# Kernel tuning notes

Measured on AMD Instinct MI355X. Metric: run time of the kernel, lower is better.

The kernel has to match this reference:

```python
import jax, jax.numpy as jnp
import numpy as np

WS = 7       # window_size
SS = 3       # shift_size
HEADS = 6
HD = 32      # head_dim
DIM = 192    # embedding_dim
MLP_RATIO = 4
SCALE = HD ** -0.5
MM = WS * WS
NEG = -1e9


def _rel_index():
    # Swin relative-position index, shape [MM, MM], values in [0, (2*WS-1)^2)
    coords = np.stack(np.meshgrid(np.arange(WS), np.arange(WS), indexing='ij')).reshape(2, -1)
    rel = coords[:, :, None] - coords[:, None, :]          # [2, MM, MM]
    rel = rel.transpose(1, 2, 0).astype(np.int64)          # [MM, MM, 2]
    rel[:, :, 0] += WS - 1
    rel[:, :, 1] += WS - 1
    rel[:, :, 0] *= 2 * WS - 1
    return rel.sum(-1)                                     # [MM, MM]


def _shift_mask(h, w):
    # attention mask for shifted windows, shape [nh*nw, MM, MM]
    img = np.zeros((h, w), dtype=np.float32)
    cnt = 0
    for hs in (slice(0, -WS), slice(-WS, -SS), slice(-SS, None)):
        for ws_ in (slice(0, -WS), slice(-WS, -SS), slice(-SS, None)):
            img[hs, ws_] = cnt
            cnt += 1
    mw = img.reshape(h // WS, WS, w // WS, WS).transpose(0, 2, 1, 3).reshape(-1, MM)
    diff = mw[:, None, :] - mw[:, :, None]
    return np.where(diff != 0, NEG, 0.0).astype(np.float32)


def _ln(x, g, b):
    m = x.mean(-1, keepdims=True)
    v = ((x - m) ** 2).mean(-1, keepdims=True)
    return (x - m) / jnp.sqrt(v + 1e-5) * g + b


def setup_inputs() -> dict:
    key = jax.random.key(0)
    ks = jax.random.split(key, 8)
    inner = HEADS * HD

    def n(k, shape, s=0.02):
        return jax.random.normal(k, shape, jnp.float32) * s

    return {
        'x': jax.random.normal(ks[0], (64, DIM, 56, 56), jnp.float32),
        'ln1_g': jnp.ones((DIM,), jnp.float32),
        'ln1_b': jnp.zeros((DIM,), jnp.float32),
        'qkv_w': n(ks[1], (3 * inner, DIM)),
        'out_w': n(ks[2], (DIM, inner)),
        'out_b': jnp.zeros((DIM,), jnp.float32),
        'ln2_g': jnp.ones((DIM,), jnp.float32),
        'ln2_b': jnp.zeros((DIM,), jnp.float32),
        'mlp_w1': n(ks[3], (MLP_RATIO * DIM, DIM)),
        'mlp_b1': jnp.zeros((MLP_RATIO * DIM,), jnp.float32),
        'mlp_w2': n(ks[4], (DIM, MLP_RATIO * DIM)),
        'mlp_b2': jnp.zeros((DIM,), jnp.float32),
        'rel_table': n(ks[5], ((2 * WS - 1) ** 2, HEADS)),
    }


def reference(x, ln1_g, ln1_b, qkv_w, out_w, out_b, ln2_g, ln2_b,
              mlp_w1, mlp_b1, mlp_w2, mlp_b2, rel_table):
    b, c, h, w = x.shape
    nh, nw = h // WS, w // WS

    # cyclic shift
    xs = jnp.roll(x, (-SS, -SS), axis=(2, 3))
    # window partition: [b,c,h,w] -> [b*nh*nw, MM, c]
    xw = (xs.reshape(b, c, nh, WS, nw, WS)
            .transpose(0, 2, 4, 3, 5, 1)
            .reshape(b * nh * nw, MM, c))

    # --- attention (PreNorm) ---
    y = _ln(xw, ln1_g, ln1_b)
    qkv = y @ qkv_w.T                                 # [Bw, MM, 3*inner]
    q, k, v = jnp.split(qkv, 3, axis=-1)

    def to_heads(t):
        return t.reshape(-1, MM, HEADS, HD).transpose(0, 2, 1, 3)  # [Bw,H,MM,HD]

    q, k, v = to_heads(q), to_heads(k), to_heads(v)
    logits = jnp.einsum('bhid,bhjd->bhij', q, k) * SCALE           # [Bw,H,MM,MM]

    idx = jnp.asarray(_rel_index())
    bias = rel_table[idx.reshape(-1)].reshape(MM, MM, HEADS).transpose(2, 0, 1)  # [H,MM,MM]
    smask = jnp.asarray(_shift_mask(h, w))                         # [nh*nw,MM,MM]

    logits = (logits.reshape(b, nh * nw, HEADS, MM, MM)
              + bias[None, None] + smask[None, :, None])
    attn = jax.nn.softmax(logits, axis=-1).reshape(b * nh * nw, HEADS, MM, MM)
    o = jnp.einsum('bhij,bhjd->bhid', attn, v)                     # [Bw,H,MM,HD]
    o = o.transpose(0, 2, 1, 3).reshape(-1, MM, HEADS * HD)
    xw = xw + o @ out_w.T + out_b

    # --- MLP (PreNorm) ---
    y = _ln(xw, ln2_g, ln2_b)
    xw = xw + jax.nn.gelu(y @ mlp_w1.T + mlp_b1, approximate=False) @ mlp_w2.T + mlp_b2

    # window reverse + reverse shift
    xr = (xw.reshape(b, nh, nw, WS, WS, c)
            .transpose(0, 5, 1, 3, 2, 4)
            .reshape(b, c, h, w))
    return jnp.roll(xr, (SS, SS), axis=(2, 3))
```

## Files before the change

### kernel.cpp

```cpp
#include <hip/hip_runtime.h>
#include <hip/hip_bf16.h>
#include <hip/hip_fp8.h>

typedef unsigned short u16;
typedef unsigned int u32;
typedef unsigned char u8;
typedef __attribute__((ext_vector_type(4))) float fx4;
typedef __attribute__((ext_vector_type(8))) __bf16 bf8;

#define NEGV -1e9f
#define LOG2E 1.4426950408889634f
#define SCALE2 (0.17677669529663687f*1.4426950408889634f)

static __device__ __forceinline__ u16 f2bu(float f){
    __hip_bfloat16 h = __float2bfloat16(f);
    return *reinterpret_cast<u16*>(&h);
}
static __device__ __forceinline__ float b2f(u16 u){
    __hip_bfloat16 h;
    *reinterpret_cast<u16*>(&h) = u;
    return __bfloat162float(h);
}
static __device__ __forceinline__ u8 f2f8(float v){
    __hip_fp8_e4m3 t(v);
    return *reinterpret_cast<u8*>(&t);
}
static __device__ __forceinline__ float frcp(float x){
#if __has_builtin(__builtin_amdgcn_rcpf)
    return __builtin_amdgcn_rcpf(x);
#else
    return 1.f/x;
#endif
}
static __device__ __forceinline__ float frsq(float x){
#if __has_builtin(__builtin_amdgcn_rsqf)
    return __builtin_amdgcn_rsqf(x);
#else
    return rsqrtf(x);
#endif
}
static __device__ __forceinline__ float gelu_f(float v){
    return v * frcp(1.f + __builtin_amdgcn_exp2f(-2.4554418f*v));
}

__global__ __launch_bounds__(256) void f2b2_kernel(
        const float* __restrict__ s1, const float* __restrict__ s3,
        u16* __restrict__ d1, u8* __restrict__ d3){
    int i = blockIdx.x*256 + threadIdx.x;
    if (i < 36864)  d1[i] = f2bu(s1[i]);
    if (i < 147456) d3[i] = f2f8(s3[i]*16.f);
}

__global__ __launch_bounds__(256) void wprep_kernel(
        const float* __restrict__ qkv_w, const float* __restrict__ g1, const float* __restrict__ b1,
        const float* __restrict__ w1,    const float* __restrict__ g2, const float* __restrict__ b2,
        const float* __restrict__ mb1,
        u16* __restrict__ WqP, float* __restrict__ wsq, float* __restrict__ ccq,
        u16* __restrict__ W1P, float* __restrict__ ws1, float* __restrict__ cc1){
    const int row = blockIdx.x*4 + (threadIdx.x>>6);
    const int l = threadIdx.x & 63;
    const int isq = row < 576;
    const int n = isq ? row : row - 576;
    if (row >= 1344) return;
    const float* src = (isq ? qkv_w : w1) + (size_t)n*192;
    const float* g = isq ? g1 : g2;
    const float* b = isq ? b1 : b2;
    u16* dst = (isq ? WqP : W1P) + (size_t)n*192;
    float sw = 0.f, sc = 0.f;
    #pragma unroll
    for (int t=0;t<3;t++){
        const int k = l + t*64;
        const float wv = src[k];
        const float wp = wv*g[k];
        dst[k] = f2bu(wp);
        sw += wp; sc += b[k]*wv;
    }
    #pragma unroll
    for (int o=32;o;o>>=1){ sw += __shfl_xor(sw,o,64); sc += __shfl_xor(sc,o,64); }
    if (!l){
        if (isq){ wsq[n]=sw; ccq[n]=sc; }
        else    { ws1[n]=sw; cc1[n]=sc + mb1[n]; }
    }
}

__global__ __launch_bounds__(256) void ltab_kernel(const float* __restrict__ rel_table,
                                                   float* __restrict__ LT){
    const int blk = blockIdx.x;
    const int cls = blk/6, h = blk - cls*6;
    float* T = LT + blk*4096;
    for (int e = threadIdx.x; e < 4096; e += 256){
        const int i = e>>6, j = e&63;
        float v = NEGV;
        if (i < 49 && j < 49){
            const int id = i/7, im = i-id*7, jd = j/7, jm = j-jd*7;
            const int ridx = (id-jd+6)*13 + (im-jm+6);
            const float bias = rel_table[ridx*6 + h];
            const int ri = (cls&2) ? (id<4?1:2) : 0;
            const int rj = (cls&2) ? (jd<4?1:2) : 0;
            const int ci = (cls&1) ? (im<4?1:2) : 0;
            const int cj = (cls&1) ? (jm<4?1:2) : 0;
            v = bias + ((ri==rj && ci==cj) ? 0.f : NEGV);
        }
        T[e] = v * LOG2E;
    }
}

__global__ __launch_bounds__(256) void partition_ln_kernel(
        const float* __restrict__ x, u16* __restrict__ xw, float2* __restrict__ RS1){
    __shared__ float lds[192*57];
    const int bi = blockIdx.x;
    const int b = bi/56, i = bi%56;
    const int si = (i+3)%56;
    const float* src = x + (size_t)b*602112 + (size_t)si*56;
    for (int e = threadIdx.x; e < 10752; e += 256){
        int c = e/56, j = e%56;
        lds[c*57 + j] = src[(size_t)c*3136 + j];
    }
    __syncthreads();
    const int wrow_base = (b*8 + i/7)*8;
    const int prow = (i%7)*7;
    for (int e = threadIdx.x; e < 10752; e += 256){
        int j = e/192, c = e%192;
        int t = (wrow_base + j/7)*49 + prow + (j%7);
        xw[(size_t)t*192 + c] = f2bu(lds[c*57 + (j+3)%56]);
    }
    const int wv = threadIdx.x>>6, l = threadIdx.x&63;
    for (int j = wv; j < 56; j += 4){
        const int jj = (j+3)%56;
        float v0 = lds[l*57 + jj], v1 = lds[(l+64)*57 + jj], v2 = lds[(l+128)*57 + jj];
        float s = v0+v1+v2;
        #pragma unroll
        for (int o=32;o;o>>=1) s += __shfl_xor(s, o, 64);
        const float mean = s*(1.f/192.f);
        float d0 = v0-mean, d1 = v1-mean, d2 = v2-mean;
        float qv = d0*d0 + d1*d1 + d2*d2;
        #pragma unroll
        for (int o=32;o;o>>=1) qv += __shfl_xor(qv, o, 64);
        const float rstd = frsq(qv*(1.f/192.f) + 1e-5f);
        if (l == 0){
            const int t = (wrow_base + j/7)*49 + prow + (j%7);
            RS1[t] = make_float2(mean, rstd);
        }
    }
}

__global__ __launch_bounds__(256) void reverse_kernel(const u16* __restrict__ xw, float* __restrict__ out){
    __shared__ float lds[192*57];
    const int bi = blockIdx.x;
    const int b = bi/56, h = bi%56;
    const int i = (h+53)%56;
    const int wrow_base = (b*8 + i/7)*8;
    const int prow = (i%7)*7;
    for (int e = threadIdx.x; e < 10752; e += 256){
        int j = e/192, c = e%192;
        int t = (wrow_base + j/7)*49 + prow + (j%7);
        lds[c*57 + j] = b2f(xw[(size_t)t*192 + c]);
    }
    __syncthreads();
    float* dst = out + (size_t)b*602112 + (size_t)h*56;
    for (int e = threadIdx.x; e < 10752; e += 256){
        int c = e/56, w = e%56;
        dst[(size_t)c*3136 + w] = lds[c*57 + (w+53)%56];
    }
}

template<int ROWS>
static __device__ __forceinline__ void stage_tile(const char* __restrict__ g, size_t row0,
                                                  int kc, int pitch, u16* ldsbase, int tid){
    const int w = tid>>6, lane = tid&63;
    const int sub = lane>>3;
    const int b16 = (lane&7) ^ sub;
    #pragma unroll
    for (int i=0; i<ROWS/32; ++i){
        const int row = i*32 + w*8 + sub;
        const char* src = g + (row0+row)*(size_t)pitch + (size_t)kc*128 + b16*16;
        u16* dst = ldsbase + i*2048 + w*512;
#if __has_builtin(__builtin_amdgcn_global_load_lds)
        __builtin_amdgcn_global_load_lds(
            (const __attribute__((address_space(1))) u32*)src,
            (__attribute__((address_space(3))) u32*)dst, 16, 0, 0);
#else
        *(uint4*)(dst + lane*8) = *(const uint4*)src;
#endif
    }
}

static __device__ __forceinline__ bf8 rd_frag16(const u16* lds, int row, int boff){
    const char* p = (const char*)lds + row*128 + (boff ^ ((row&7)<<4));
    return *(const bf8*)p;
}
static __device__ __forceinline__ long rd_frag8(const u16* lds, int row, int boff){
    const char* p = (const char*)lds + row*128 + (boff ^ ((row&7)<<4));
    return *(const long*)p;
}

template<int KEL,int ESZ,int NY,int NTOT,int ACT,int RES,int LNF,int STATS,int OUT,int HASB>
__global__ __launch_bounds__(256,2) void gemm_kernel(
    const void* __restrict__ Av, const void* __restrict__ Bv,
    const float* __restrict__ bias, const u16* __restrict__ res,
    void* __restrict__ out,
    const float2* __restrict__ RSin, const float* __restrict__ wsum,
    const float* __restrict__ cc, float2* __restrict__ RSout,
    float ascale)
{
    constexpr int NKT = (KEL*ESZ)/128;
    constexpr int KKS = (ESZ==1)?4:2;
    constexpr int PITCH = KEL*ESZ;
    __shared__ __align__(16) u16 lds[40960];
    const int tid = threadIdx.x;
    const int wv = tid>>6, l = tid&63, lr = l&15, lg = l>>4;
    const int wm = wv&1, wn = wv>>1;
    const int chunk = gridDim.x >> 3;
    const int orig = (blockIdx.x & 7)*chunk + (blockIdx.x >> 3);
    const int mt = orig / NY;
    const int nc = orig - mt*NY;
    const size_t row0 = (size_t)mt*128;
    const int n0 = nc*192;
    const char* A = (const char*)Av;
    const char* Bblk = (const char*)Bv + (size_t)n0*PITCH;

    stage_tile<128>(A, row0, 0, PITCH, lds, tid);
    stage_tile<192>(Bblk, 0, 0, PITCH, lds+16384, tid);
    __syncthreads();

    fx4 acc[4][6] = {};
    for (int kc=0; kc<NKT; ++kc){
        const int cur = kc & 1;
        u16* Ac = cur ? (u16*)lds+8192  : (u16*)lds;
        u16* Bc = cur ? (u16*)lds+28672 : (u16*)lds+16384;
        if (kc+1 < NKT){
            u16* An = cur ? (u16*)lds       : (u16*)lds+8192;
            u16* Bn = cur ? (u16*)lds+16384 : (u16*)lds+28672;
            stage_tile<128>(A, row0, kc+1, PITCH, An, tid);
            stage_tile<192>(Bblk, 0, kc+1, PITCH, Bn, tid);
        }
        #pragma unroll
        for (int kk=0; kk<KKS; ++kk){
            if constexpr (ESZ==2){
                bf8 af[4], bfr[6];
                #pragma unroll
                for (int r=0;r<4;r++) af[r]  = rd_frag16(Ac, wm*64 + r*16 + lr, kk*64 + lg*16);
                #pragma unroll
                for (int c=0;c<6;c++) bfr[c] = rd_frag16(Bc, wn*96 + c*16 + lr, kk*64 + lg*16);
                #pragma unroll
                for (int r=0;r<4;r++)
                    #pragma unroll
                    for (int c=0;c<6;c++)
                        acc[r][c] = __builtin_amdgcn_mfma_f32_16x16x32_bf16(af[r], bfr[c], acc[r][c], 0,0,0);
            } else {
                long af[4], bfr[6];
                #pragma unroll
                for (int r=0;r<4;r++) af[r]  = rd_frag8(Ac, wm*64 + r*16 + lr, kk*32 + lg*8);
                #pragma unroll
                for (int c=0;c<6;c++) bfr[c] = rd_frag8(Bc, wn*96 + c*16 + lr, kk*32 + lg*8);
                #pragma unroll
                for (int r=0;r<4;r++)
                    #pragma unroll
                    for (int c=0;c<6;c++)
                        acc[r][c] = __builtin_amdgcn_mfma_f32_16x16x32_fp8_fp8(af[r], bfr[c], acc[r][c], 0,0,0);
            }
        }
        __syncthreads();
    }

    float sA[4][4], sB[4][4];
    if constexpr (LNF){
        #pragma unroll
        for (int r=0;r<4;r++)
            #pragma unroll
            for (int q=0;q<4;q++){
                const float2 st = RSin[row0 + wm*64 + r*16 + lg*4 + q];
                sA[r][q] = st.y;
                sB[r][q] = -st.x*st.y;
            }
    }
    float ss[4][4], ss2[4][4];
    if constexpr (STATS){
        #pragma unroll
        for (int r=0;r<4;r++)
            #pragma unroll
            for (int q=0;q<4;q++){ ss[r][q]=0.f; ss2[r][q]=0.f; }
    }
    #pragma unroll
    for (int c=0;c<6;c++){
        const int col = n0 + wn*96 + c*16 + lr;
        float bv = 0.f, wsc = 0.f, ccc = 0.f;
        if constexpr (HASB) bv = bias[col];
        if constexpr (LNF){ wsc = wsum[col]; ccc = cc[col]; }
        #pragma unroll
        for (int r=0;r<4;r++){
            const size_t grow0 = row0 + wm*64 + r*16 + lg*4;
            float vq[4];
            #pragma unroll
            for (int q=0;q<4;q++){
                float v = acc[r][c][q];
                if constexpr (ESZ==1) v *= ascale;
                if constexpr (LNF) v = fmaf(v, sA[r][q], fmaf(sB[r][q], wsc, ccc));
                else v += bv;
                if constexpr (ACT) v = gelu_f(v);
                if constexpr (RES) v += b2f(res[(grow0+q)*NTOT + col]);
                if constexpr (STATS){ ss[r][q] += v; ss2[r][q] += v*v; }
                vq[q] = v;
            }
            if constexpr (OUT==1){
                u16* ob = (u16*)out + grow0*NTOT + col;
                ob[0] = f2bu(vq[0]);
                ob[NTOT] = f2bu(vq[1]);
                ob[2*NTOT] = f2bu(vq[2]);
                ob[3*NTOT] = f2bu(vq[3]);
            } else {
                u8* ob = (u8*)out + grow0*(size_t)NTOT + col;
#if __has_builtin(__builtin_amdgcn_cvt_pk_fp8_f32)
                const u32 p01 = (u32)__builtin_amdgcn_cvt_pk_fp8_f32(vq[0], vq[1], 0, false);
                const u32 p23 = (u32)__builtin_amdgcn_cvt_pk_fp8_f32(vq[2], vq[3], 0, false);
                ob[0] = (u8)p01;
                ob[NTOT] = (u8)(p01>>8);
                ob[2*NTOT] = (u8)p23;
                ob[3*NTOT] = (u8)(p23>>8);
#else
                ob[0] = f2f8(vq[0]);
                ob[NTOT] = f2f8(vq[1]);
                ob[2*NTOT] = f2f8(vq[2]);
                ob[3*NTOT] = f2f8(vq[3]);
#endif
            }
        }
    }
    if constexpr (STATS){
        float* redS = (float*)lds;
        #pragma unroll
        for (int r=0;r<4;r++)
            #pragma unroll
            for (int q=0;q<4;q++){
                float s = ss[r][q], s2 = ss2[r][q];
                #pragma unroll
                for (int o=8;o;o>>=1){ s += __shfl_xor(s, o, 64); s2 += __shfl_xor(s2, o, 64); }
                if (lr == 0){
                    const int rowl = wm*64 + r*16 + lg*4 + q;
                    redS[(wn*128 + rowl)*2 + 0] = s;
                    redS[(wn*128 + rowl)*2 + 1] = s2;
                }
            }
        __syncthreads();
        for (int row = tid; row < 128; row += 256){
            const float S  = redS[row*2+0] + redS[(128+row)*2+0];
            const float S2 = redS[row*2+1] + redS[(128+row)*2+1];
            const float mean = S*(1.f/192.f);
            const float rstd = frsq(S2*(1.f/192.f) - mean*mean + 1e-5f);
            RSout[row0 + row] = make_float2(mean, rstd);
        }
    }
}

__global__ __launch_bounds__(64) void attn_kernel(const u16* __restrict__ qkv,
                                                  const float* __restrict__ LT,
                                                  u16* __restrict__ o)
{
    __shared__ u16 pa[64*64];
    __shared__ u16 vt[32*64];
    const int bid = blockIdx.x;
    const int widx = bid/6, h = bid - widx*6;
    const int wi = widx & 63;
    const int nhi = wi>>3, nwi = wi&7;
    const int l = threadIdx.x, lr = l&15, lg = l>>4;
    const u16* base = qkv + (size_t)widx*49*576;
    const int cls = ((nhi==7)?2:0) | ((nwi==7)?1:0);
    const float* Th = LT + (size_t)(cls*6 + h)*4096;

    bf8 qf[4], kf[4];
    #pragma unroll
    for (int t=0;t<4;t++){
        const int row = min(t*16 + lr, 48);
        qf[t] = *(const bf8*)(base + (size_t)row*576 + h*32 + lg*8);
        kf[t] = *(const bf8*)(base + (size_t)row*576 + 192 + h*32 + lg*8);
    }
    for (int e=l; e<480; e+=64){
        int d = e/15, j = 49 + (e - d*15);
        vt[d*64 + (j ^ ((d&7)<<3))] = 0;
    }
    for (int e=l; e<784; e+=64){
        int j = e>>4, dp = e&15;
        u32 val = *(const u32*)(base + (size_t)j*576 + 384 + h*32 + dp*2);
        const int d0 = dp*2, d1 = dp*2+1;
        vt[d0*64 + (j ^ ((d0&7)<<3))] = (u16)(val & 0xffffu);
        vt[d1*64 + (j ^ ((d1&7)<<3))] = (u16)(val >> 16);
    }

    fx4 acc[4][4] = {};
    #pragma unroll
    for (int ti=0;ti<4;ti++)
        #pragma unroll
        for (int tj=0;tj<4;tj++)
            acc[ti][tj] = __builtin_amdgcn_mfma_f32_16x16x32_bf16(qf[ti], kf[tj], acc[ti][tj], 0,0,0);

    #pragma unroll
    for (int ti=0;ti<4;ti++){
        #pragma unroll
        for (int reg=0;reg<4;reg++){
            const int i = ti*16 + lg*4 + reg;
            const float* rowp = Th + i*64;
            #pragma unroll
            for (int tj=0;tj<4;tj++)
                acc[ti][tj][reg] = fmaf(acc[ti][tj][reg], SCALE2, rowp[tj*16 + lr]);
        }
    }
    #pragma unroll
    for (int ti=0;ti<4;ti++){
        #pragma unroll
        for (int reg=0;reg<4;reg++){
            float mx = fmaxf(fmaxf(acc[ti][0][reg], acc[ti][1][reg]),
                             fmaxf(acc[ti][2][reg], acc[ti][3][reg]));
            #pragma unroll
            for (int o2=8;o2;o2>>=1) mx = fmaxf(mx, __shfl_xor(mx, o2, 64));
            float sum = 0.f;
            #pragma unroll
            for (int tj=0;tj<4;tj++){
                float p = __builtin_amdgcn_exp2f(acc[ti][tj][reg] - mx);
                acc[ti][tj][reg] = p;
                sum += p;
            }
            #pragma unroll
            for (int o2=8;o2;o2>>=1) sum += __shfl_xor(sum, o2, 64);
            const float rs = frcp(sum);
            #pragma unroll
            for (int tj=0;tj<4;tj++) acc[ti][tj][reg] *= rs;
        }
    }
    #pragma unroll
    for (int ti=0;ti<4;ti++)
        #pragma unroll
        for (int tj=0;tj<4;tj++)
            #pragma unroll
            for (int reg=0;reg<4;reg++){
                const int row = ti*16 + lg*4 + reg;
                pa[row*64 + ((tj*16+lr) ^ ((row&7)<<3))] = f2bu(acc[ti][tj][reg]);
            }
    __syncthreads();

    fx4 oacc[4][2] = {};
    #pragma unroll
    for (int kk=0;kk<2;kk++){
        bf8 bfr[2];
        #pragma unroll
        for (int cd=0;cd<2;cd++){
            const int rowb = cd*16 + lr;
            bfr[cd] = *(const bf8*)(vt + rowb*64 + ((kk*32 + lg*8) ^ ((rowb&7)<<3)));
        }
        #pragma unroll
        for (int ti=0;ti<4;ti++){
            const int rowa = ti*16 + lr;
            bf8 afr = *(const bf8*)(pa + rowa*64 + ((kk*32 + lg*8) ^ ((rowa&7)<<3)));
            #pragma unroll
            for (int cd=0;cd<2;cd++)
                oacc[ti][cd] = __builtin_amdgcn_mfma_f32_16x16x32_bf16(afr, bfr[cd], oacc[ti][cd], 0,0,0);
        }
    }
    u16* ob = o + (size_t)widx*49*192 + h*32;
    #pragma unroll
    for (int ti=0;ti<4;ti++)
        #pragma unroll
        for (int cd=0;cd<2;cd++)
            #pragma unroll
            for (int q=0;q<4;q++){
                const int i = ti*16 + lg*4 + q;
                if (i < 49) ob[(size_t)i*192 + cd*16 + lr] = f2bu(oacc[ti][cd][q]);
            }
}

extern "C" void kernel_launch(void* const* d_in, const int* in_sizes, int n_in,
                              void* d_out, int out_size, void* d_ws, size_t ws_size,
                              hipStream_t stream)
{
    const float* x      = (const float*)d_in[0];
    const float* ln1_g  = (const float*)d_in[1];
    const float* ln1_b  = (const float*)d_in[2];
    const float* qkv_w  = (const float*)d_in[3];
    const float* out_w  = (const float*)d_in[4];
    const float* out_b  = (const float*)d_in[5];
    const float* ln2_g  = (const float*)d_in[6];
    const float* ln2_b  = (const float*)d_in[7];
    const float* mlp_w1 = (const float*)d_in[8];
    const float* mlp_b1 = (const float*)d_in[9];
    const float* mlp_w2 = (const float*)d_in[10];
    const float* mlp_b2 = (const float*)d_in[11];
    const float* rel_t  = (const float*)d_in[12];

    char* ws = (char*)d_ws;
    u16*    Ybuf  = (u16*)ws;
    float*  LTab  = (float*)(ws + 77070336);
    float2* RS1   = (float2*)(ws + 77600000);
    float2* RS2   = (float2*)(ws + 79300000);
    u16*    WqP   = (u16*)(ws + 81000000);
    float*  wsq   = (float*)(ws + 81300000);
    float*  ccq   = (float*)(ws + 81310000);
    u16*    W1P   = (u16*)(ws + 81400000);
    float*  ws1   = (float*)(ws + 81700000);
    float*  cc1   = (float*)(ws + 81710000);
    u16*    XWbuf = (u16*)(ws + 154140672);
    u16*    QKVH  = (u16*)(ws + 231211008);
    u8*     Hbuf  = (u8*)(ws + 231211008);
    u16*    Wo    = (u16*)(ws + 539492352);
    u8*     W2f8  = (u8*)(ws + 539492352 + 73728);

    f2b2_kernel<<<576,256,0,stream>>>(out_w, mlp_w2, Wo, W2f8);
    wprep_kernel<<<336,256,0,stream>>>(qkv_w, ln1_g, ln1_b, mlp_w1, ln2_g, ln2_b, mlp_b1,
                                       WqP, wsq, ccq, W1P, ws1, cc1);
    ltab_kernel<<<24,256,0,stream>>>(rel_t, LTab);

    partition_ln_kernel<<<3584,256,0,stream>>>(x, XWbuf, RS1);
    gemm_kernel<192,2,3,576,0,0,1,0,1,0><<<4704,256,0,stream>>>(
        XWbuf, WqP, nullptr, nullptr, QKVH, RS1, wsq, ccq, nullptr, 1.f);
    attn_kernel<<<24576,64,0,stream>>>(QKVH, LTab, Ybuf);
    gemm_kernel<192,2,1,192,0,1,0,1,1,1><<<1568,256,0,stream>>>(
        Ybuf, Wo, out_b, XWbuf, XWbuf, nullptr, nullptr, nullptr, RS2, 1.f);
    gemm_kernel<192,2,4,768,1,0,1,0,2,0><<<6272,256,0,stream>>>(
        XWbuf, W1P, nullptr, nullptr, Hbuf, RS2, ws1, cc1, nullptr, 1.f);
    gemm_kernel<768,1,1,192,0,1,0,0,1,1><<<1568,256,0,stream>>>(
        Hbuf, W2f8, mlp_b2, XWbuf, Ybuf, nullptr, nullptr, nullptr, nullptr, 0.0625f);
    reverse_kernel<<<3584,256,0,stream>>>(Ybuf, (float*)d_out);
}
```

Baseline: 692.6 us.

## Reorder logit bias table to lane layout, defer softmax normalization, shrink LDS

Rewrites the precomputed log-bias/mask table so that each lane reads its MFMA accumulator positions as contiguous float4 loads instead of scattered scalar loads. Softmax normalization is moved after the PV matmul, scaling the output rows by the reciprocal sum instead of scaling every probability. The P buffer in LDS is shrunk to 50 rows with clamped reads, and the V-transpose swizzle is changed to reduce bank conflicts. Together these cut global load instructions, ALU multiplies and LDS footprint in the attention kernel, at the cost of rounding unnormalized probabilities to bf16, which slightly changes numerics.

```diff
diff --git a/kernel.cpp b/kernel.cpp
--- a/kernel.cpp
+++ b/kernel.cpp
@@ -89,7 +89,11 @@
     const int cls = blk/6, h = blk - cls*6;
     float* T = LT + blk*4096;
     for (int e = threadIdx.x; e < 4096; e += 256){
-        const int i = e>>6, j = e&63;
+        const int lane = e>>6, rem = e&63;
+        const int ti = rem>>4, reg = (rem>>2)&3, tj = rem&3;
+        const int lg = lane>>4, lr = lane&15;
+        const int i = ti*16 + lg*4 + reg;
+        const int j = tj*16 + lr;
         float v = NEGV;
         if (i < 49 && j < 49){
             const int id = i/7, im = i-id*7, jd = j/7, jm = j-jd*7;
@@ -356,7 +360,7 @@
                                                   const float* __restrict__ LT,
                                                   u16* __restrict__ o)
 {
-    __shared__ u16 pa[64*64];
+    __shared__ u16 pa[50*64];
     __shared__ u16 vt[32*64];
     const int bid = blockIdx.x;
     const int widx = bid/6, h = bid - widx*6;
@@ -365,7 +369,7 @@
     const int l = threadIdx.x, lr = l&15, lg = l>>4;
     const u16* base = qkv + (size_t)widx*49*576;
     const int cls = ((nhi==7)?2:0) | ((nwi==7)?1:0);
-    const float* Th = LT + (size_t)(cls*6 + h)*4096;
+    const float* Ths = LT + (size_t)(cls*6 + h)*4096 + l*64;
 
     bf8 qf[4], kf[4];
     #pragma unroll
@@ -376,14 +380,14 @@
     }
     for (int e=l; e<480; e+=64){
         int d = e/15, j = 49 + (e - d*15);
-        vt[d*64 + (j ^ ((d&7)<<3))] = 0;
+        vt[d*64 + (j ^ (((d>>1)&7)<<3))] = 0;
     }
     for (int e=l; e<784; e+=64){
         int j = e>>4, dp = e&15;
         u32 val = *(const u32*)(base + (size_t)j*576 + 384 + h*32 + dp*2);
-        const int d0 = dp*2, d1 = dp*2+1;
-        vt[d0*64 + (j ^ ((d0&7)<<3))] = (u16)(val & 0xffffu);
-        vt[d1*64 + (j ^ ((d1&7)<<3))] = (u16)(val >> 16);
+        const int d0 = dp*2, d1 = d0+1;
+        vt[d0*64 + (j ^ ((dp&7)<<3))] = (u16)(val & 0xffffu);
+        vt[d1*64 + (j ^ ((dp&7)<<3))] = (u16)(val >> 16);
     }
 
     fx4 acc[4][4] = {};
@@ -397,13 +401,13 @@
     for (int ti=0;ti<4;ti++){
         #pragma unroll
         for (int reg=0;reg<4;reg++){
-            const int i = ti*16 + lg*4 + reg;
-            const float* rowp = Th + i*64;
+            const fx4 lt = *(const fx4*)(Ths + ti*16 + reg*4);
             #pragma unroll
             for (int tj=0;tj<4;tj++)
-                acc[ti][tj][reg] = fmaf(acc[ti][tj][reg], SCALE2, rowp[tj*16 + lr]);
-        }
-    }
+                acc[ti][tj][reg] = fmaf(acc[ti][tj][reg], SCALE2, lt[tj]);
+        }
+    }
+    float sums[4][4];
     #pragma unroll
     for (int ti=0;ti<4;ti++){
         #pragma unroll
@@ -421,9 +425,7 @@
             }
             #pragma unroll
             for (int o2=8;o2;o2>>=1) sum += __shfl_xor(sum, o2, 64);
-            const float rs = frcp(sum);
-            #pragma unroll
-            for (int tj=0;tj<4;tj++) acc[ti][tj][reg] *= rs;
+            sums[ti][reg] = sum;
         }
     }
     #pragma unroll
@@ -433,7 +435,8 @@
             #pragma unroll
             for (int reg=0;reg<4;reg++){
                 const int row = ti*16 + lg*4 + reg;
-                pa[row*64 + ((tj*16+lr) ^ ((row&7)<<3))] = f2bu(acc[ti][tj][reg]);
+                if (row < 50)
+                    pa[row*64 + ((tj*16+lr) ^ ((row&7)<<3))] = f2bu(acc[ti][tj][reg]);
             }
     __syncthreads();
 
@@ -444,11 +447,11 @@
         #pragma unroll
         for (int cd=0;cd<2;cd++){
             const int rowb = cd*16 + lr;
-            bfr[cd] = *(const bf8*)(vt + rowb*64 + ((kk*32 + lg*8) ^ ((rowb&7)<<3)));
+            bfr[cd] = *(const bf8*)(vt + rowb*64 + ((kk*32 + lg*8) ^ (((rowb>>1)&7)<<3)));
         }
         #pragma unroll
         for (int ti=0;ti<4;ti++){
-            const int rowa = ti*16 + lr;
+            const int rowa = min(ti*16 + lr, 49);
             bf8 afr = *(const bf8*)(pa + rowa*64 + ((kk*32 + lg*8) ^ ((rowa&7)<<3)));
             #pragma unroll
             for (int cd=0;cd<2;cd++)
@@ -457,14 +460,18 @@
     }
     u16* ob = o + (size_t)widx*49*192 + h*32;
     #pragma unroll
-    for (int ti=0;ti<4;ti++)
+    for (int ti=0;ti<4;ti++){
+        float rsv[4];
+        #pragma unroll
+        for (int q=0;q<4;q++) rsv[q] = frcp(sums[ti][q]);
         #pragma unroll
         for (int cd=0;cd<2;cd++)
             #pragma unroll
             for (int q=0;q<4;q++){
                 const int i = ti*16 + lg*4 + q;
-                if (i < 49) ob[(size_t)i*192 + cd*16 + lr] = f2bu(oacc[ti][cd][q]);
-            }
+                if (i < 49) ob[(size_t)i*192 + cd*16 + lr] = f2bu(oacc[ti][cd][q]*rsv[q]);
+            }
+    }
 }
 
 extern "C" void kernel_launch(void* const* d_in, const int* in_sizes, int n_in,
```

Measured after the change: 687.2 us. About the same (-0.8%).
